# Kernel tuning notes

Measured on AMD Instinct MI355X. Metric: run time of the kernel, lower is better.

## Reference

```python
import jax, jax.numpy as jnp
import numpy as np
from jax import lax

N = 50000          # fluid particles
E = 1_600_000      # radius-graph edges (avg degree 32)
F_IN = 4           # fluidFeatures
NB = 8             # n = m = 8 basis functions per axis
K = NB * NB        # 64 total basis functions
SUPPORT = 1.0      # attributes['support']
LAYERS = [32, 64, 64, 2]


def setup_inputs() -> dict:
    key = jax.random.key(0)
    ks = jax.random.split(key, 24)
    inp = {
        "fluidPositions": jax.random.uniform(ks[0], (N, 2), jnp.float32),
        "fluidFeatures": jax.random.normal(ks[1], (N, F_IN), jnp.float32),
        "edge_i": jax.random.randint(ks[2], (E,), 0, N),  # receiver
        "edge_j": jax.random.randint(ks[3], (E,), 0, N),  # sender
    }
    # conv in/out channels per RbfNet wiring (boundaryFeatures == 0):
    dims = [(F_IN, LAYERS[0]), (2 * LAYERS[0], LAYERS[1]), (LAYERS[1], LAYERS[2]), (LAYERS[2], LAYERS[3])]
    k = 4
    for idx, (ci, co) in enumerate(dims):
        inp[f"cw{idx}"] = 0.1 * jax.random.normal(ks[k], (K, ci, co), jnp.float32); k += 1
        inp[f"cb{idx}"] = jnp.zeros((co,), jnp.float32)
        inp[f"fw{idx}"] = 0.1 * jax.random.normal(ks[k], (ci, co), jnp.float32); k += 1
        inp[f"fb{idx}"] = jnp.zeros((co,), jnp.float32)
    return inp


def _linear_basis(x, n):
    # hat (linear) RBF basis on n uniformly spaced centers in [-1, 1]
    centers = jnp.linspace(-1.0, 1.0, n, dtype=x.dtype)
    spacing = 2.0 / (n - 1)
    return jnp.maximum(0.0, 1.0 - jnp.abs(x[:, None] - centers[None, :]) / spacing)  # [E, n]


def _edge_basis(pos, ei, ej):
    # fluidEdgeLengths = -(pos[j] - pos[i]) / support, clamped to [-1, 1]
    d = (pos[ei] - pos[ej]) / SUPPORT
    d = jnp.clip(d, -1.0, 1.0)
    mask = ei != ej  # centerIgnore: drop self edges
    d = jnp.where(mask[:, None], d, jnp.array([1.0, 0.0], d.dtype))  # keep atan2 grads finite
    r = jnp.sqrt(jnp.sum(d * d, axis=-1) + 1e-12)
    u = jnp.clip(2.0 * r - 1.0, -1.0, 1.0)          # polar mapping: radius -> [-1, 1]
    v = jnp.arctan2(d[:, 1], d[:, 0]) / jnp.pi       # polar mapping: angle  -> [-1, 1]
    bu = _linear_basis(u, NB)
    bv = _linear_basis(v, NB)
    basis = (bu[:, :, None] * bv[:, None, :]).reshape(ei.shape[0], K)  # separable 2D basis
    return basis * mask[:, None].astype(basis.dtype)


def _rbf_conv(x, ei, ej, basis, W, b):
    # out[i] = sum_{e: dst(e)=i} sum_k basis[e,k] * (x[src(e)] @ W[k]) + b
    xj = x[ej]                           # [E, Cin] neighbor gather
    n_nodes = x.shape[0]
    init = jnp.zeros((n_nodes, W.shape[-1]), x.dtype)
    def body(acc, kw):
        bk, Wk = kw                      # bk: [E], Wk: [Cin, Cout]
        mom = jax.ops.segment_sum(bk[:, None] * xj, ei, num_segments=n_nodes)  # [N, Cin]
        return acc + mom @ Wk, None
    out, _ = lax.scan(body, init, (basis.T, W))
    return out + b


def reference(fluidPositions, fluidFeatures, edge_i, edge_j,
              cw0, cb0, fw0, fb0, cw1, cb1, fw1, fb1,
              cw2, cb2, fw2, fb2, cw3, cb3, fw3, fb3):
    basis = _edge_basis(fluidPositions, edge_i, edge_j)
    # layer 0: dense branch + fluid continuous conv, hstacked
    lin0 = fluidFeatures @ fw0 + fb0
    conv0 = _rbf_conv(fluidFeatures, edge_i, edge_j, basis, cw0, cb0)
    ans = jnp.concatenate([lin0, conv0], axis=1)  # [N, 64]
    # layer 1: features 32 != 64 -> no residual
    a = jax.nn.relu(ans)
    ans = _rbf_conv(a, edge_i, edge_j, basis, cw1, cb1) + a @ fw1 + fb1
    # layer 2: features 64 == 64 -> residual add
    a = jax.nn.relu(ans)
    ans = _rbf_conv(a, edge_i, edge_j, basis, cw2, cb2) + a @ fw2 + fb2 + ans
    # layer 3: features 64 != 2 -> no residual
    a = jax.nn.relu(ans)
    ans = _rbf_conv(a, edge_i, edge_j, basis, cw3, cb3) + a @ fw3 + fb3
    return ans / 128.0
```

## Files before the change

### kernel.cpp

```cpp
#include <hip/hip_runtime.h>
#include <math.h>

typedef _Float16 h8 __attribute__((ext_vector_type(8)));
typedef _Float16 h2 __attribute__((ext_vector_type(2)));
typedef float f32x4 __attribute__((ext_vector_type(4)));

__device__ __forceinline__ float clampf(float x, float lo, float hi) {
    return fminf(fmaxf(x, lo), hi);
}

__global__ void zero_ints(int* __restrict__ p, int n) {
    int i = blockIdx.x * 256 + threadIdx.x;
    if (i < n) p[i] = 0;
}

__global__ void repack_wh(const float* __restrict__ cw, const float* __restrict__ fw,
                          _Float16* __restrict__ Wh) {
    int idx = blockIdx.x * 256 + threadIdx.x;
    int total = 4 * 130 * 512;
    if (idx >= total) return;
    int j8 = idx & 7;
    int l = (idx >> 3) & 63;
    int rest = idx >> 9;
    int s = rest % 130;
    int t = rest / 130;
    int p = s * 32 + ((l >> 4) * 8) + j8;
    int co = t * 16 + (l & 15);
    float v = 0.f;
    if (p < 4096) {
        int tile = p >> 8;
        int g = (p >> 6) & 3;
        int m = (p >> 2) & 15;
        int i = p & 3;
        int mt = tile >> 2;
        int ct = tile & 3;
        int bin = mt * 16 + g * 4 + i;
        int c = ct * 16 + m;
        v = cw[(bin * 64 + c) * 64 + co];
    } else if (p < 4160) {
        v = fw[(p - 4096) * 64 + co];
    }
    Wh[idx] = (_Float16)v;
}

__global__ void edge_hist(const int* __restrict__ ei, const int* __restrict__ ej,
                          int* __restrict__ counts, int E) {
    int e = blockIdx.x * 256 + threadIdx.x;
    if (e >= E) return;
    int i = ei[e], j = ej[e];
    if (i != j) atomicAdd(&counts[i], 1);
}

__global__ __launch_bounds__(1024) void scan_kernel(const int* __restrict__ counts,
                                                    int* __restrict__ offs,
                                                    int* __restrict__ cursor, int N) {
    __shared__ int sums[1024];
    const int t = threadIdx.x;
    const int per = (N + 1023) / 1024;
    const int lo = t * per;
    const int hi = min(lo + per, N);
    int s = 0;
    for (int i = lo; i < hi; ++i) s += counts[i];
    sums[t] = s;
    __syncthreads();
    for (int d = 1; d < 1024; d <<= 1) {
        int v = (t >= d) ? sums[t - d] : 0;
        __syncthreads();
        sums[t] += v;
        __syncthreads();
    }
    int run = (t > 0) ? sums[t - 1] : 0;
    for (int i = lo; i < hi; ++i) {
        offs[i] = run;
        cursor[i] = run;
        run += counts[i];
    }
    if (t == 1023) offs[N] = sums[1023];
}

__global__ void edge_scatter(const int* __restrict__ ei, const int* __restrict__ ej,
                             const float* __restrict__ pos, int* __restrict__ cursor,
                             uint4* __restrict__ csr_all, int E) {
    int e = blockIdx.x * 256 + threadIdx.x;
    if (e >= E) return;
    int i = ei[e], j = ej[e];
    if (i == j) return;
    float dx = clampf(pos[i * 2 + 0] - pos[j * 2 + 0], -1.f, 1.f);
    float dy = clampf(pos[i * 2 + 1] - pos[j * 2 + 1], -1.f, 1.f);
    float r = sqrtf(dx * dx + dy * dy + 1e-12f);
    float u = clampf(2.f * r - 1.f, -1.f, 1.f);
    float v = atan2f(dy, dx) * 0.3183098861837907f;
    float tu = (u + 1.f) * 3.5f;
    float tv = (v + 1.f) * 3.5f;
    int iu = min(6, max(0, (int)floorf(tu)));
    int iv = min(6, max(0, (int)floorf(tv)));
    float fu = clampf(tu - (float)iu, 0.f, 1.f);
    float fv = clampf(tv - (float)iv, 0.f, 1.f);
    bool even = (iu & 1) == 0;
    int rowi0 = even ? iu : iu + 1;
    int rowi1 = even ? iu + 1 : iu;
    float wu0 = even ? (1.f - fu) : fu;
    float wu1 = even ? fu : (1.f - fu);
    float gv = 1.f - fv;
    int ivd = iv >> 1;
    unsigned o0 = (unsigned)(rowi0 * 256 + ivd * 64);
    unsigned o1 = (unsigned)(rowi1 * 256 + ivd * 64);
    unsigned offp = o0 | (o1 << 11) | ((unsigned)(iv & 1) << 22);
    unsigned a0 = (unsigned)__builtin_bit_cast(unsigned short, (_Float16)(wu0 * gv)) |
                  ((unsigned)__builtin_bit_cast(unsigned short, (_Float16)(wu0 * fv)) << 16);
    unsigned a1 = (unsigned)__builtin_bit_cast(unsigned short, (_Float16)(wu1 * gv)) |
                  ((unsigned)__builtin_bit_cast(unsigned short, (_Float16)(wu1 * fv)) << 16);
    int p = atomicAdd(&cursor[i], 1);
    csr_all[p] = make_uint4(
        (unsigned)j | ((unsigned)(rowi0 >> 1) << 17) | ((unsigned)(rowi1 >> 1) << 19) |
            ((unsigned)iv << 21),
        offp, a0, a1);
}

template <int MODE>
__global__ __launch_bounds__(1024, 4) void conv64_mfma(
    const _Float16* __restrict__ xh, const float* __restrict__ x32,
    const _Float16* __restrict__ Wh,
    const float* __restrict__ cb, const float* __restrict__ fb,
    const int* __restrict__ offs, const uint4* __restrict__ csr_all,
    float* __restrict__ out32, _Float16* __restrict__ xh_out, int nNodes) {
    constexpr int TM = 16;
    constexpr int KSTEPS = 130;
    constexpr int RSH = 4168;
    extern __shared__ _Float16 smem[];
    const int tid = threadIdx.x;
    const int w = tid >> 6;
    const int lane = tid & 63;
    const int base = blockIdx.x * TM;
    const int n = base + w;

    _Float16* Ast = smem + w * RSH;
    _Float16* Bst = Ast + 2048;

    f32x4 acc[16] = {{0, 0, 0, 0}, {0, 0, 0, 0}, {0, 0, 0, 0}, {0, 0, 0, 0},
                     {0, 0, 0, 0}, {0, 0, 0, 0}, {0, 0, 0, 0}, {0, 0, 0, 0},
                     {0, 0, 0, 0}, {0, 0, 0, 0}, {0, 0, 0, 0}, {0, 0, 0, 0},
                     {0, 0, 0, 0}, {0, 0, 0, 0}, {0, 0, 0, 0}, {0, 0, 0, 0}};

    if (n < nNodes) {
        const int e0 = offs[n], e1 = offs[n + 1];
        const int half = lane >> 5;
        const int el = lane & 31;
        for (int bs = e0; bs < e1; bs += 32) {
            {
                uint4 z4 = make_uint4(0, 0, 0, 0);
#pragma unroll
                for (int zz = 0; zz < 4; ++zz) ((uint4*)Ast)[zz * 64 + lane] = z4;
            }
            int e = bs + el;
            bool ok = e < e1;
            uint4 ca = csr_all[ok ? e : e0];
            int jme = ok ? (int)(ca.x & 0x1FFFF) : -1;
            {
                int iv = (ca.x >> 21) & 7;
                int rowi = half ? (int)((((ca.x >> 19) & 3) << 1) + 1)
                                : (int)(((ca.x >> 17) & 3) << 1);
                h2 wts = __builtin_bit_cast(h2, half ? ca.w : ca.z);
                if (ok) {
                    int bin0 = rowi * 8 + iv;
                    int bin1 = bin0 + 1;
                    int a0 = bin0 * 32 + (((el >> 3) + (bin0 >> 1)) & 3) * 8 + (el & 7);
                    int a1 = bin1 * 32 + (((el >> 3) + (bin1 >> 1)) & 3) * 8 + (el & 7);
                    Ast[a0] = wts[0];
                    Ast[a1] = wts[1];
                }
            }
#pragma unroll
            for (int it = 0; it < 4; ++it) {
                int ee = it * 8 + (lane >> 3);
                int jj = __shfl(jme, ee);
                int c0 = (lane & 7) * 8;
                uint4 bv = make_uint4(0, 0, 0, 0);
                if (jj >= 0) bv = *(const uint4*)(xh + (size_t)jj * 64 + c0);
                int sub = (ee >> 2) * 4 + (c0 >> 4);
                int row = (ee & 3) ^ it;
                ((uint4*)Bst)[sub * 8 + row * 2 + ((c0 >> 3) & 1)] = bv;
            }
            h8 bf[4];
#pragma unroll
            for (int ct = 0; ct < 4; ++ct) {
                h8 b;
#pragma unroll
                for (int jj2 = 0; jj2 < 8; ++jj2) {
                    int ee = (lane >> 4) * 8 + jj2;
                    int addr = ((ee >> 2) * 4 + ct) * 64 + ((ee & 3) ^ (lane >> 4)) * 16 +
                               (lane & 15);
                    b[jj2] = Bst[addr];
                }
                bf[ct] = b;
            }
#pragma unroll
            for (int mt = 0; mt < 4; ++mt) {
                int binr = mt * 16 + (lane & 15);
                int aoff = binr * 32 + (((lane >> 4) + (binr >> 1)) & 3) * 8;
                h8 a = *(const h8*)(Ast + aoff);
#pragma unroll
                for (int ct = 0; ct < 4; ++ct)
                    acc[mt * 4 + ct] = __builtin_amdgcn_mfma_f32_16x16x32_f16(
                        a, bf[ct], acc[mt * 4 + ct], 0, 0, 0);
            }
        }
#pragma unroll
        for (int t = 0; t < 16; ++t) {
            h2 lo = {(_Float16)acc[t][0], (_Float16)acc[t][1]};
            h2 hi = {(_Float16)acc[t][2], (_Float16)acc[t][3]};
            h2* dst = (h2*)(smem + w * RSH + t * 256 + (lane >> 4) * 64 + (lane & 15) * 4);
            dst[0] = lo;
            dst[1] = hi;
        }
        smem[w * RSH + 4096 + lane] = xh[(size_t)n * 64 + lane];
    }

    const int s0 = w * 8 + min(w, 2);
    const int s_end = s0 + 8 + (w < 2 ? 1 : 0);
    const int quad = lane >> 4;
    const _Float16* arow = smem + (lane & 15) * RSH;

    const uint4* Bp = (const uint4*)Wh;
    uint4 b0[4], b1[4];
#pragma unroll
    for (int t = 0; t < 4; ++t) {
        b0[t] = Bp[((size_t)t * KSTEPS + s0) * 64 + lane];
        b1[t] = Bp[((size_t)t * KSTEPS + s0 + 1) * 64 + lane];
    }
    __syncthreads();
    f32x4 acc2[4] = {{0, 0, 0, 0}, {0, 0, 0, 0}, {0, 0, 0, 0}, {0, 0, 0, 0}};
    for (int s = s0; s < s_end; ++s) {
        uint4 bq[4];
#pragma unroll
        for (int t = 0; t < 4; ++t) {
            bq[t] = b0[t];
            b0[t] = b1[t];
            if (s + 2 < s_end) b1[t] = Bp[((size_t)t * KSTEPS + s + 2) * 64 + lane];
        }
        h8 a = *(const h8*)(arow + s * 32 + quad * 8);
#pragma unroll
        for (int t = 0; t < 4; ++t)
            acc2[t] = __builtin_amdgcn_mfma_f32_16x16x32_f16(a, __builtin_bit_cast(h8, bq[t]),
                                                             acc2[t], 0, 0, 0);
    }
    __syncthreads();
    f32x4* red = (f32x4*)smem;
#pragma unroll
    for (int t = 0; t < 4; ++t) red[(w * 4 + t) * 64 + lane] = acc2[t];
    __syncthreads();
    if (w < 4) {
        f32x4 s = {0, 0, 0, 0};
#pragma unroll
        for (int g = 0; g < 16; ++g) s += red[(g * 4 + w) * 64 + lane];
        const int co = w * 16 + (lane & 15);
#pragma unroll
        for (int i = 0; i < 4; ++i) {
            int nn = base + quad * 4 + i;
            if (nn < nNodes) {
                float res = s[i] + cb[co] + fb[co];
                if (MODE == 2) res += x32[(size_t)nn * 64 + co];
                out32[(size_t)nn * 64 + co] = res;
                if (MODE == 1) xh_out[(size_t)nn * 64 + co] = (_Float16)fmaxf(res, 0.f);
            }
        }
    }
}

__global__ __launch_bounds__(1024, 4) void conv_last(
    const float* __restrict__ x, const float* __restrict__ cw3, const float* __restrict__ fw3,
    const float* __restrict__ cb3, const float* __restrict__ fb3,
    const int* __restrict__ offs, const uint4* __restrict__ csr_all,
    float* __restrict__ out, int nNodes) {
    constexpr int TM = 16;
    __shared__ float2 W2[4096];
    __shared__ float2 FW2[64];
    const int tid = threadIdx.x;
    const int w = tid >> 6;
    const int lane = tid & 63;
    const int base = blockIdx.x * TM;
    const int n = base + w;

    {
        const float2* src = (const float2*)cw3;
        for (int d = tid; d < 4096; d += 1024) W2[d] = src[d];
        if (tid < 64) FW2[tid] = ((const float2*)fw3)[tid];
    }
    __syncthreads();

    float2 acc = make_float2(0.f, 0.f);
    if (n < nNodes) {
        const int e0 = offs[n], e1 = offs[n + 1];
        const int c = lane;
        for (int b = e0; b < e1; b += 4) {
            uint4 ca[4];
            float xv[4];
#pragma unroll
            for (int u = 0; u < 4; ++u) {
                int e = b + u;
                bool ok = e < e1;
                ca[u] = csr_all[ok ? e : e0];
                xv[u] = ok ? 1.f : 0.f;
            }
#pragma unroll
            for (int u = 0; u < 4; ++u) {
                int j = ca[u].x & 0x1FFFF;
                xv[u] *= fmaxf(x[j * 64 + c], 0.f);
            }
#pragma unroll
            for (int u = 0; u < 4; ++u) {
                int r0 = ((ca[u].x >> 17) & 3) << 1;
                int r1 = (((ca[u].x >> 19) & 3) << 1) + 1;
                int iv = (ca[u].x >> 21) & 7;
                h2 wh0 = __builtin_bit_cast(h2, ca[u].z);
                h2 wh1 = __builtin_bit_cast(h2, ca[u].w);
                float w00 = (float)wh0[0], w01 = (float)wh0[1];
                float w10 = (float)wh1[0], w11 = (float)wh1[1];
                int b00 = (r0 * 8 + iv) * 64 + c;
                int b10 = (r1 * 8 + iv) * 64 + c;
                float2 t00 = W2[b00], t01 = W2[b00 + 64];
                float2 t10 = W2[b10], t11 = W2[b10 + 64];
                float wsx = w00 * t00.x + w01 * t01.x + w10 * t10.x + w11 * t11.x;
                float wsy = w00 * t00.y + w01 * t01.y + w10 * t10.y + w11 * t11.y;
                acc.x += xv[u] * wsx;
                acc.y += xv[u] * wsy;
            }
        }
        float xr = fmaxf(x[n * 64 + c], 0.f);
        float2 fwp = FW2[c];
        acc.x += xr * fwp.x;
        acc.y += xr * fwp.y;
    }
#pragma unroll
    for (int d = 1; d < 64; d <<= 1) {
        acc.x += __shfl_xor(acc.x, d);
        acc.y += __shfl_xor(acc.y, d);
    }
    if (lane == 0 && n < nNodes) {
        out[n * 2 + 0] = (acc.x + cb3[0] + fb3[0]) * (1.f / 128.f);
        out[n * 2 + 1] = (acc.y + cb3[1] + fb3[1]) * (1.f / 128.f);
    }
}

__global__ __launch_bounds__(1024, 4) void conv0_direct(
    const float* __restrict__ x, const float* __restrict__ cw0, const float* __restrict__ fw0,
    const float* __restrict__ cb0, const float* __restrict__ fb0,
    const int* __restrict__ offs, const uint4* __restrict__ csr_all,
    _Float16* __restrict__ out, int nNodes) {
    constexpr int TM = 16;
    __shared__ float2 W0p[4096];
    __shared__ float2 FW0p[64];
    const int tid = threadIdx.x;
    const int w = tid >> 6;
    const int lane = tid & 63;
    const int base = blockIdx.x * TM;
    const int n = base + w;

    {
        for (int d = tid; d < 4096; d += 1024) {
            int co = d & 31;
            int h = (d >> 5) & 1;
            int bin = d >> 6;
            W0p[d] = make_float2(cw0[(bin * 4 + 2 * h) * 32 + co],
                                 cw0[(bin * 4 + 2 * h + 1) * 32 + co]);
        }
        if (tid < 64) {
            int co = tid & 31;
            int h = tid >> 5;
            FW0p[tid] = make_float2(fw0[(2 * h) * 32 + co], fw0[(2 * h + 1) * 32 + co]);
        }
    }
    __syncthreads();

    const int co = lane & 31;
    const int h = lane >> 5;
    float accC = 0.f, accL = 0.f;
    if (n < nNodes) {
        const int e0 = offs[n], e1 = offs[n + 1];
        for (int b = e0; b < e1; b += 4) {
            uint4 ca[4];
            float xc0[4], xc1[4];
#pragma unroll
            for (int u = 0; u < 4; ++u) {
                int e = b + u;
                bool ok = e < e1;
                ca[u] = csr_all[ok ? e : e0];
                xc0[u] = ok ? 1.f : 0.f;
            }
#pragma unroll
            for (int u = 0; u < 4; ++u) {
                int j = ca[u].x & 0x1FFFF;
                const float4 xj = *(const float4*)(x + j * 4);
                float a = h ? xj.z : xj.x;
                float bb = h ? xj.w : xj.y;
                xc1[u] = xc0[u] * bb;
                xc0[u] = xc0[u] * a;
            }
#pragma unroll
            for (int u = 0; u < 4; ++u) {
                int r0 = ((ca[u].x >> 17) & 3) << 1;
                int r1 = (((ca[u].x >> 19) & 3) << 1) + 1;
                int iv = (ca[u].x >> 21) & 7;
                h2 wh0 = __builtin_bit_cast(h2, ca[u].z);
                h2 wh1 = __builtin_bit_cast(h2, ca[u].w);
                float w00 = (float)wh0[0], w01 = (float)wh0[1];
                float w10 = (float)wh1[0], w11 = (float)wh1[1];
                int i00 = ((r0 * 8 + iv) * 2 + h) * 32 + co;
                int i10 = ((r1 * 8 + iv) * 2 + h) * 32 + co;
                float2 t00 = W0p[i00], t01 = W0p[i00 + 64];
                float2 t10 = W0p[i10], t11 = W0p[i10 + 64];
                accC += w00 * (xc0[u] * t00.x + xc1[u] * t00.y);
                accC += w01 * (xc0[u] * t01.x + xc1[u] * t01.y);
                accC += w10 * (xc0[u] * t10.x + xc1[u] * t10.y);
                accC += w11 * (xc0[u] * t11.x + xc1[u] * t11.y);
            }
        }
        const float4 xn = *(const float4*)(x + n * 4);
        float a = h ? xn.z : xn.x;
        float bb = h ? xn.w : xn.y;
        float2 fwp = FW0p[h * 32 + co];
        accL = a * fwp.x + bb * fwp.y;
    }
    accC += __shfl_xor(accC, 32);
    accL += __shfl_xor(accL, 32);
    if (lane < 32 && n < nNodes) {
        out[n * 64 + co] = (_Float16)fmaxf(accL + fb0[co], 0.f);
        out[n * 64 + 32 + co] = (_Float16)fmaxf(accC + cb0[co], 0.f);
    }
}

extern "C" void kernel_launch(void* const* d_in, const int* in_sizes, int n_in,
                              void* d_out, int out_size, void* d_ws, size_t ws_size,
                              hipStream_t stream) {
    const float* pos = (const float*)d_in[0];
    const float* feat = (const float*)d_in[1];
    const int* ei = (const int*)d_in[2];
    const int* ej = (const int*)d_in[3];
    const float* cw0 = (const float*)d_in[4];
    const float* cb0 = (const float*)d_in[5];
    const float* fw0 = (const float*)d_in[6];
    const float* fb0 = (const float*)d_in[7];
    const float* cw1 = (const float*)d_in[8];
    const float* cb1 = (const float*)d_in[9];
    const float* fw1 = (const float*)d_in[10];
    const float* fb1 = (const float*)d_in[11];
    const float* cw2 = (const float*)d_in[12];
    const float* cb2 = (const float*)d_in[13];
    const float* fw2 = (const float*)d_in[14];
    const float* fb2 = (const float*)d_in[15];
    const float* cw3 = (const float*)d_in[16];
    const float* cb3 = (const float*)d_in[17];
    const float* fw3 = (const float*)d_in[18];
    const float* fb3 = (const float*)d_in[19];
    float* outp = (float*)d_out;

    const int N = in_sizes[0] / 2;
    const int E = in_sizes[2];

    char* wsp = (char*)d_ws;
    size_t off = 0;
    auto alloc = [&](size_t bytes) -> void* {
        void* p = wsp + off;
        off = (off + bytes + 255) & ~(size_t)255;
        return p;
    };
    int* counts = (int*)alloc((size_t)N * 4);
    int* offs = (int*)alloc((size_t)(N + 1) * 4);
    int* cursor = (int*)alloc((size_t)N * 4);
    uint4* csr_all = (uint4*)alloc((size_t)E * 16);
    float* ansA = (float*)alloc((size_t)N * 64 * 4);
    float* ansB = (float*)alloc((size_t)N * 64 * 4);
    _Float16* xhB = (_Float16*)alloc((size_t)N * 64 * 2);
    _Float16* Wh1 = (_Float16*)alloc((size_t)4 * 130 * 512 * 2);
    _Float16* Wh2 = (_Float16*)alloc((size_t)4 * 130 * 512 * 2);
    _Float16* xh0 = (_Float16*)ansA;
    (void)ws_size;
    (void)n_in;
    (void)out_size;

    const int BIG_LDS = 16 * 4168 * 2;
    hipFuncSetAttribute((const void*)&conv64_mfma<1>,
                        hipFuncAttributeMaxDynamicSharedMemorySize, BIG_LDS);
    hipFuncSetAttribute((const void*)&conv64_mfma<2>,
                        hipFuncAttributeMaxDynamicSharedMemorySize, BIG_LDS);

    zero_ints<<<dim3((N + 255) / 256), dim3(256), 0, stream>>>(counts, N);
    const int RT = 4 * 130 * 512;
    repack_wh<<<dim3((RT + 255) / 256), dim3(256), 0, stream>>>(cw1, fw1, Wh1);
    repack_wh<<<dim3((RT + 255) / 256), dim3(256), 0, stream>>>(cw2, fw2, Wh2);
    edge_hist<<<dim3((E + 255) / 256), dim3(256), 0, stream>>>(ei, ej, counts, E);
    scan_kernel<<<dim3(1), dim3(1024), 0, stream>>>(counts, offs, cursor, N);
    edge_scatter<<<dim3((E + 255) / 256), dim3(256), 0, stream>>>(ei, ej, pos, cursor, csr_all, E);

    const int nb = (N + 15) / 16;
    conv0_direct<<<dim3(nb), dim3(1024), 0, stream>>>(
        feat, cw0, fw0, cb0, fb0, offs, csr_all, xh0, N);
    conv64_mfma<1><<<dim3(nb), dim3(1024), BIG_LDS, stream>>>(
        xh0, (const float*)nullptr, Wh1, cb1, fb1, offs, csr_all, ansB, xhB, N);
    conv64_mfma<2><<<dim3(nb), dim3(1024), BIG_LDS, stream>>>(
        xhB, ansB, Wh2, cb2, fb2, offs, csr_all, ansA, (_Float16*)nullptr, N);
    conv_last<<<dim3(nb), dim3(1024), 0, stream>>>(
        ansA, cw3, fw3, cb3, fb3, offs, csr_all, outp, N);
}
```

Before: 915.3 us.

## Move first and last conv layers onto MFMA gather-then-GEMM path

Replaces the scalar direct-accumulation kernels for layer 0 and the final layer with MFMA-based kernels. Each builds per-node basis moments in LDS via matrix ops, then multiplies by repacked fp16 weights, with a block-level reduction across waves. Layer 2 now emits fp16 post-ReLU activations instead of fp32, so the last layer gathers half the bytes per neighbour. The edge record drops its unused offset word. In exchange the final layer runs in fp16 with mostly-padded 16-wide output tiles, and two more weight repack launches are added.

Measured after the change: 856.8 us. 6.4% less time.

```diff
diff --git a/kernel.cpp b/kernel.cpp
--- a/kernel.cpp
+++ b/kernel.cpp
@@ -43,6 +43,59 @@
     Wh[idx] = (_Float16)v;
 }
 
+__global__ void repack_wh3(const float* __restrict__ cw, const float* __restrict__ fw,
+                           _Float16* __restrict__ Wh) {
+    int idx = blockIdx.x * 256 + threadIdx.x;
+    int total = 130 * 512;
+    if (idx >= total) return;
+    int j8 = idx & 7;
+    int l = (idx >> 3) & 63;
+    int s = idx >> 9;
+    int p = s * 32 + ((l >> 4) * 8) + j8;
+    int co = l & 15;
+    float v = 0.f;
+    if (co < 2) {
+        if (p < 4096) {
+            int tile = p >> 8;
+            int g = (p >> 6) & 3;
+            int m = (p >> 2) & 15;
+            int i = p & 3;
+            int mt = tile >> 2;
+            int ct = tile & 3;
+            int bin = mt * 16 + g * 4 + i;
+            int c = ct * 16 + m;
+            v = cw[(bin * 64 + c) * 2 + co];
+        } else if (p < 4160) {
+            v = fw[(p - 4096) * 2 + co];
+        }
+    }
+    Wh[idx] = (_Float16)v;
+}
+
+__global__ void repack_w0h(const float* __restrict__ cw0, const float* __restrict__ fw0,
+                           _Float16* __restrict__ Wh) {
+    int idx = blockIdx.x * 256 + threadIdx.x;
+    int total = 4 * 9 * 512;
+    if (idx >= total) return;
+    int j8 = idx & 7;
+    int l = (idx >> 3) & 63;
+    int rest = idx >> 9;
+    int s = rest % 9;
+    int t = rest / 9;
+    int p = s * 32 + ((l >> 4) * 8) + j8;
+    int co = t * 16 + (l & 15);
+    float v = 0.f;
+    if (p < 256) {
+        int bin = p & 63;
+        int c = p >> 6;
+        if (co >= 32) v = cw0[(bin * 4 + c) * 32 + (co - 32)];
+    } else if (p < 260) {
+        int c = p - 256;
+        if (co < 32) v = fw0[c * 32 + co];
+    }
+    Wh[idx] = (_Float16)v;
+}
+
 __global__ void edge_hist(const int* __restrict__ ei, const int* __restrict__ ej,
                           int* __restrict__ counts, int E) {
     int e = blockIdx.x * 256 + threadIdx.x;
@@ -102,10 +155,6 @@
     float wu0 = even ? (1.f - fu) : fu;
     float wu1 = even ? fu : (1.f - fu);
     float gv = 1.f - fv;
-    int ivd = iv >> 1;
-    unsigned o0 = (unsigned)(rowi0 * 256 + ivd * 64);
-    unsigned o1 = (unsigned)(rowi1 * 256 + ivd * 64);
-    unsigned offp = o0 | (o1 << 11) | ((unsigned)(iv & 1) << 22);
     unsigned a0 = (unsigned)__builtin_bit_cast(unsigned short, (_Float16)(wu0 * gv)) |
                   ((unsigned)__builtin_bit_cast(unsigned short, (_Float16)(wu0 * fv)) << 16);
     unsigned a1 = (unsigned)__builtin_bit_cast(unsigned short, (_Float16)(wu1 * gv)) |
@@ -114,7 +163,85 @@
     csr_all[p] = make_uint4(
         (unsigned)j | ((unsigned)(rowi0 >> 1) << 17) | ((unsigned)(rowi1 >> 1) << 19) |
             ((unsigned)iv << 21),
-        offp, a0, a1);
+        0u, a0, a1);
+}
+
+__device__ __forceinline__ void mom_phase1_64(
+    const _Float16* __restrict__ xh, const uint4* __restrict__ csr_all,
+    _Float16* Ast, _Float16* Bst, int e0, int e1, int lane, f32x4* acc) {
+    const int half = lane >> 5;
+    const int el = lane & 31;
+    for (int bs = e0; bs < e1; bs += 32) {
+        {
+            uint4 z4 = make_uint4(0, 0, 0, 0);
+#pragma unroll
+            for (int zz = 0; zz < 4; ++zz) ((uint4*)Ast)[zz * 64 + lane] = z4;
+        }
+        int e = bs + el;
+        bool ok = e < e1;
+        uint4 ca = csr_all[ok ? e : e0];
+        int jme = ok ? (int)(ca.x & 0x1FFFF) : -1;
+        {
+            int iv = (ca.x >> 21) & 7;
+            int rowi = half ? (int)((((ca.x >> 19) & 3) << 1) + 1)
+                            : (int)(((ca.x >> 17) & 3) << 1);
+            h2 wts = __builtin_bit_cast(h2, half ? ca.w : ca.z);
+            if (ok) {
+                int bin0 = rowi * 8 + iv;
+                int bin1 = bin0 + 1;
+                int a0 = bin0 * 32 + (((el >> 3) + (bin0 >> 1)) & 3) * 8 + (el & 7);
+                int a1 = bin1 * 32 + (((el >> 3) + (bin1 >> 1)) & 3) * 8 + (el & 7);
+                Ast[a0] = wts[0];
+                Ast[a1] = wts[1];
+            }
+        }
+#pragma unroll
+        for (int it = 0; it < 4; ++it) {
+            int ee = it * 8 + (lane >> 3);
+            int jj = __shfl(jme, ee);
+            int c0 = (lane & 7) * 8;
+            uint4 bv = make_uint4(0, 0, 0, 0);
+            if (jj >= 0) bv = *(const uint4*)(xh + (size_t)jj * 64 + c0);
+            int sub = (ee >> 2) * 4 + (c0 >> 4);
+            int row = (ee & 3) ^ it;
+            ((uint4*)Bst)[sub * 8 + row * 2 + ((c0 >> 3) & 1)] = bv;
+        }
+        h8 bf[4];
+#pragma unroll
+        for (int ct = 0; ct < 4; ++ct) {
+            h8 b;
+#pragma unroll
+            for (int jj2 = 0; jj2 < 8; ++jj2) {
+                int ee = (lane >> 4) * 8 + jj2;
+                int addr = ((ee >> 2) * 4 + ct) * 64 + ((ee & 3) ^ (lane >> 4)) * 16 +
+                           (lane & 15);
+                b[jj2] = Bst[addr];
+            }
+            bf[ct] = b;
+        }
+#pragma unroll
+        for (int mt = 0; mt < 4; ++mt) {
+            int binr = mt * 16 + (lane & 15);
+            int aoff = binr * 32 + (((lane >> 4) + (binr >> 1)) & 3) * 8;
+            h8 a = *(const h8*)(Ast + aoff);
+#pragma unroll
+            for (int ct = 0; ct < 4; ++ct)
+                acc[mt * 4 + ct] = __builtin_amdgcn_mfma_f32_16x16x32_f16(
+                    a, bf[ct], acc[mt * 4 + ct], 0, 0, 0);
+        }
+    }
+}
+
+__device__ __forceinline__ void mom_writeback_64(const f32x4* acc, _Float16* momrow,
+                                                 int lane) {
+#pragma unroll
+    for (int t = 0; t < 16; ++t) {
+        h2 lo = {(_Float16)acc[t][0], (_Float16)acc[t][1]};
+        h2 hi = {(_Float16)acc[t][2], (_Float16)acc[t][3]};
+        h2* dst = (h2*)(momrow + t * 256 + (lane >> 4) * 64 + (lane & 15) * 4);
+        dst[0] = lo;
+        dst[1] = hi;
+    }
 }
 
 template <int MODE>
@@ -126,7 +253,7 @@
     float* __restrict__ out32, _Float16* __restrict__ xh_out, int nNodes) {
     constexpr int TM = 16;
     constexpr int KSTEPS = 130;
-    constexpr int RSH = 4168;
+    constexpr int RSH = 4184;
     extern __shared__ _Float16 smem[];
     const int tid = threadIdx.x;
     const int w = tid >> 6;
@@ -141,6 +268,146 @@
                      {0, 0, 0, 0}, {0, 0, 0, 0}, {0, 0, 0, 0}, {0, 0, 0, 0},
                      {0, 0, 0, 0}, {0, 0, 0, 0}, {0, 0, 0, 0}, {0, 0, 0, 0},
                      {0, 0, 0, 0}, {0, 0, 0, 0}, {0, 0, 0, 0}, {0, 0, 0, 0}};
+
+    if (n < nNodes) {
+        mom_phase1_64(xh, csr_all, Ast, Bst, offs[n], offs[n + 1], lane, acc);
+        mom_writeback_64(acc, smem + w * RSH, lane);
+        smem[w * RSH + 4096 + lane] = xh[(size_t)n * 64 + lane];
+    }
+
+    const int s0 = w * 8 + min(w, 2);
+    const int s_end = s0 + 8 + (w < 2 ? 1 : 0);
+    const int quad = lane >> 4;
+    const _Float16* arow = smem + (lane & 15) * RSH;
+
+    const uint4* Bp = (const uint4*)Wh;
+    uint4 b0[4], b1[4];
+#pragma unroll
+    for (int t = 0; t < 4; ++t) {
+        b0[t] = Bp[((size_t)t * KSTEPS + s0) * 64 + lane];
+        b1[t] = Bp[((size_t)t * KSTEPS + s0 + 1) * 64 + lane];
+    }
+    __syncthreads();
+    f32x4 acc2[4] = {{0, 0, 0, 0}, {0, 0, 0, 0}, {0, 0, 0, 0}, {0, 0, 0, 0}};
+    for (int s = s0; s < s_end; ++s) {
+        uint4 bq[4];
+#pragma unroll
+        for (int t = 0; t < 4; ++t) {
+            bq[t] = b0[t];
+            b0[t] = b1[t];
+            if (s + 2 < s_end) b1[t] = Bp[((size_t)t * KSTEPS + s + 2) * 64 + lane];
+        }
+        h8 a = *(const h8*)(arow + s * 32 + quad * 8);
+#pragma unroll
+        for (int t = 0; t < 4; ++t)
+            acc2[t] = __builtin_amdgcn_mfma_f32_16x16x32_f16(a, __builtin_bit_cast(h8, bq[t]),
+                                                             acc2[t], 0, 0, 0);
+    }
+    __syncthreads();
+    f32x4* red = (f32x4*)smem;
+#pragma unroll
+    for (int t = 0; t < 4; ++t) red[(w * 4 + t) * 64 + lane] = acc2[t];
+    __syncthreads();
+    if (w < 4) {
+        f32x4 s = {0, 0, 0, 0};
+#pragma unroll
+        for (int g = 0; g < 16; ++g) s += red[(g * 4 + w) * 64 + lane];
+        const int co = w * 16 + (lane & 15);
+#pragma unroll
+        for (int i = 0; i < 4; ++i) {
+            int nn = base + quad * 4 + i;
+            if (nn < nNodes) {
+                float res = s[i] + cb[co] + fb[co];
+                if (MODE == 2) res += x32[(size_t)nn * 64 + co];
+                if (MODE == 1) out32[(size_t)nn * 64 + co] = res;
+                xh_out[(size_t)nn * 64 + co] = (_Float16)fmaxf(res, 0.f);
+            }
+        }
+    }
+}
+
+__global__ __launch_bounds__(1024, 4) void conv_last_mfma(
+    const _Float16* __restrict__ xh, const _Float16* __restrict__ Wh3,
+    const float* __restrict__ cb3, const float* __restrict__ fb3,
+    const int* __restrict__ offs, const uint4* __restrict__ csr_all,
+    float* __restrict__ out, int nNodes) {
+    constexpr int TM = 16;
+    constexpr int RSH = 4184;
+    extern __shared__ _Float16 smem[];
+    const int tid = threadIdx.x;
+    const int w = tid >> 6;
+    const int lane = tid & 63;
+    const int base = blockIdx.x * TM;
+    const int n = base + w;
+
+    _Float16* Ast = smem + w * RSH;
+    _Float16* Bst = Ast + 2048;
+
+    f32x4 acc[16] = {{0, 0, 0, 0}, {0, 0, 0, 0}, {0, 0, 0, 0}, {0, 0, 0, 0},
+                     {0, 0, 0, 0}, {0, 0, 0, 0}, {0, 0, 0, 0}, {0, 0, 0, 0},
+                     {0, 0, 0, 0}, {0, 0, 0, 0}, {0, 0, 0, 0}, {0, 0, 0, 0},
+                     {0, 0, 0, 0}, {0, 0, 0, 0}, {0, 0, 0, 0}, {0, 0, 0, 0}};
+
+    if (n < nNodes) {
+        mom_phase1_64(xh, csr_all, Ast, Bst, offs[n], offs[n + 1], lane, acc);
+        mom_writeback_64(acc, smem + w * RSH, lane);
+        smem[w * RSH + 4096 + lane] = xh[(size_t)n * 64 + lane];
+    }
+
+    const int s0 = w * 8 + min(w, 2);
+    const int s_end = s0 + 8 + (w < 2 ? 1 : 0);
+    const int quad = lane >> 4;
+    const _Float16* arow = smem + (lane & 15) * RSH;
+    const uint4* Bp = (const uint4*)Wh3;
+
+    __syncthreads();
+    f32x4 acc2 = {0, 0, 0, 0};
+    for (int s = s0; s < s_end; ++s) {
+        uint4 bq = Bp[(size_t)s * 64 + lane];
+        h8 a = *(const h8*)(arow + s * 32 + quad * 8);
+        acc2 = __builtin_amdgcn_mfma_f32_16x16x32_f16(a, __builtin_bit_cast(h8, bq),
+                                                      acc2, 0, 0, 0);
+    }
+    __syncthreads();
+    f32x4* red = (f32x4*)smem;
+    red[w * 64 + lane] = acc2;
+    __syncthreads();
+    if (w == 0) {
+        f32x4 s = {0, 0, 0, 0};
+#pragma unroll
+        for (int g = 0; g < 16; ++g) s += red[g * 64 + lane];
+        const int co = lane & 15;
+        if (co < 2) {
+#pragma unroll
+            for (int i = 0; i < 4; ++i) {
+                int nn = base + quad * 4 + i;
+                if (nn < nNodes)
+                    out[nn * 2 + co] = (s[i] + cb3[co] + fb3[co]) * (1.f / 128.f);
+            }
+        }
+    }
+}
+
+__global__ __launch_bounds__(1024, 4) void conv0_mfma(
+    const float* __restrict__ xf, const _Float16* __restrict__ W0h,
+    const float* __restrict__ cb0, const float* __restrict__ fb0,
+    const int* __restrict__ offs, const uint4* __restrict__ csr_all,
+    _Float16* __restrict__ xh_out, int nNodes) {
+    constexpr int TM = 16;
+    constexpr int RSH0 = 296;
+    constexpr int MOMSZ = 16 * RSH0;
+    extern __shared__ _Float16 smem[];
+    const int tid = threadIdx.x;
+    const int w = tid >> 6;
+    const int lane = tid & 63;
+    const int base = blockIdx.x * TM;
+    const int n = base + w;
+
+    _Float16* Ast = smem + MOMSZ + w * 2560;
+    _Float16* Bst = Ast + 2048;
+    _Float16* momrow = smem + w * RSH0;
+
+    f32x4 acc[4] = {{0, 0, 0, 0}, {0, 0, 0, 0}, {0, 0, 0, 0}, {0, 0, 0, 0}};
 
     if (n < nNodes) {
         const int e0 = offs[n], e1 = offs[n + 1];
@@ -170,74 +437,58 @@
                     Ast[a1] = wts[1];
                 }
             }
-#pragma unroll
-            for (int it = 0; it < 4; ++it) {
-                int ee = it * 8 + (lane >> 3);
-                int jj = __shfl(jme, ee);
-                int c0 = (lane & 7) * 8;
-                uint4 bv = make_uint4(0, 0, 0, 0);
-                if (jj >= 0) bv = *(const uint4*)(xh + (size_t)jj * 64 + c0);
-                int sub = (ee >> 2) * 4 + (c0 >> 4);
-                int row = (ee & 3) ^ it;
-                ((uint4*)Bst)[sub * 8 + row * 2 + ((c0 >> 3) & 1)] = bv;
-            }
-            h8 bf[4];
-#pragma unroll
-            for (int ct = 0; ct < 4; ++ct) {
-                h8 b;
-#pragma unroll
-                for (int jj2 = 0; jj2 < 8; ++jj2) {
-                    int ee = (lane >> 4) * 8 + jj2;
-                    int addr = ((ee >> 2) * 4 + ct) * 64 + ((ee & 3) ^ (lane >> 4)) * 16 +
-                               (lane & 15);
-                    b[jj2] = Bst[addr];
-                }
-                bf[ct] = b;
+            if (half == 0) {
+                float4 xj = make_float4(0.f, 0.f, 0.f, 0.f);
+                if (jme >= 0) xj = *(const float4*)(xf + (size_t)jme * 4);
+                h2 d0 = {(_Float16)xj.x, (_Float16)xj.y};
+                h2 d1 = {(_Float16)xj.z, (_Float16)xj.w};
+                uint4 bv = make_uint4(__builtin_bit_cast(unsigned, d0),
+                                      __builtin_bit_cast(unsigned, d1), 0u, 0u);
+                uint4* dst = (uint4*)Bst + (el >> 2) * 8 + (el & 3) * 2;
+                dst[0] = bv;
+                dst[1] = make_uint4(0, 0, 0, 0);
+            }
+            h8 b;
+#pragma unroll
+            for (int jj2 = 0; jj2 < 8; ++jj2) {
+                int ee = (lane >> 4) * 8 + jj2;
+                b[jj2] = Bst[(ee >> 2) * 64 + (ee & 3) * 16 + (lane & 15)];
             }
 #pragma unroll
             for (int mt = 0; mt < 4; ++mt) {
                 int binr = mt * 16 + (lane & 15);
                 int aoff = binr * 32 + (((lane >> 4) + (binr >> 1)) & 3) * 8;
                 h8 a = *(const h8*)(Ast + aoff);
-#pragma unroll
-                for (int ct = 0; ct < 4; ++ct)
-                    acc[mt * 4 + ct] = __builtin_amdgcn_mfma_f32_16x16x32_f16(
-                        a, bf[ct], acc[mt * 4 + ct], 0, 0, 0);
-            }
-        }
-#pragma unroll
-        for (int t = 0; t < 16; ++t) {
-            h2 lo = {(_Float16)acc[t][0], (_Float16)acc[t][1]};
-            h2 hi = {(_Float16)acc[t][2], (_Float16)acc[t][3]};
-            h2* dst = (h2*)(smem + w * RSH + t * 256 + (lane >> 4) * 64 + (lane & 15) * 4);
-            dst[0] = lo;
-            dst[1] = hi;
-        }
-        smem[w * RSH + 4096 + lane] = xh[(size_t)n * 64 + lane];
-    }
-
-    const int s0 = w * 8 + min(w, 2);
-    const int s_end = s0 + 8 + (w < 2 ? 1 : 0);
+                acc[mt] = __builtin_amdgcn_mfma_f32_16x16x32_f16(a, b, acc[mt], 0, 0, 0);
+            }
+        }
+        if ((lane & 15) < 4) {
+#pragma unroll
+            for (int mt = 0; mt < 4; ++mt) {
+                _Float16* dst = momrow + mt * 16 + (lane >> 4) * 4 + 64 * (lane & 15);
+                ((h2*)dst)[0] = h2{(_Float16)acc[mt][0], (_Float16)acc[mt][1]};
+                ((h2*)dst)[1] = h2{(_Float16)acc[mt][2], (_Float16)acc[mt][3]};
+            }
+        }
+        if (lane < 7) {
+            h2 z = {(_Float16)0.f, (_Float16)0.f};
+            h2* zp = (h2*)(momrow + 260 + lane * 4);
+            zp[0] = z;
+            zp[1] = z;
+        }
+        if (lane < 4) momrow[256 + lane] = (_Float16)xf[(size_t)n * 4 + lane];
+    }
+
     const int quad = lane >> 4;
-    const _Float16* arow = smem + (lane & 15) * RSH;
-
-    const uint4* Bp = (const uint4*)Wh;
-    uint4 b0[4], b1[4];
-#pragma unroll
-    for (int t = 0; t < 4; ++t) {
-        b0[t] = Bp[((size_t)t * KSTEPS + s0) * 64 + lane];
-        b1[t] = Bp[((size_t)t * KSTEPS + s0 + 1) * 64 + lane];
-    }
+    const _Float16* arow = smem + (lane & 15) * RSH0;
+    const uint4* Bp = (const uint4*)W0h;
     __syncthreads();
     f32x4 acc2[4] = {{0, 0, 0, 0}, {0, 0, 0, 0}, {0, 0, 0, 0}, {0, 0, 0, 0}};
+    const int s0 = min(w, 9), s_end = min(w + 1, 9);
     for (int s = s0; s < s_end; ++s) {
         uint4 bq[4];
 #pragma unroll
-        for (int t = 0; t < 4; ++t) {
-            bq[t] = b0[t];
-            b0[t] = b1[t];
-            if (s + 2 < s_end) b1[t] = Bp[((size_t)t * KSTEPS + s + 2) * 64 + lane];
-        }
+        for (int t = 0; t < 4; ++t) bq[t] = Bp[((size_t)t * 9 + s) * 64 + lane];
         h8 a = *(const h8*)(arow + s * 32 + quad * 8);
 #pragma unroll
         for (int t = 0; t < 4; ++t)
@@ -245,7 +496,7 @@
                                                              acc2[t], 0, 0, 0);
     }
     __syncthreads();
-    f32x4* red = (f32x4*)smem;
+    f32x4* red = (f32x4*)(smem + MOMSZ);
 #pragma unroll
     for (int t = 0; t < 4; ++t) red[(w * 4 + t) * 64 + lane] = acc2[t];
     __syncthreads();
@@ -254,178 +505,13 @@
 #pragma unroll
         for (int g = 0; g < 16; ++g) s += red[(g * 4 + w) * 64 + lane];
         const int co = w * 16 + (lane & 15);
+        const float bias = (co < 32) ? fb0[co] : cb0[co - 32];
 #pragma unroll
         for (int i = 0; i < 4; ++i) {
             int nn = base + quad * 4 + i;
-            if (nn < nNodes) {
-                float res = s[i] + cb[co] + fb[co];
-                if (MODE == 2) res += x32[(size_t)nn * 64 + co];
-                out32[(size_t)nn * 64 + co] = res;
-                if (MODE == 1) xh_out[(size_t)nn * 64 + co] = (_Float16)fmaxf(res, 0.f);
-            }
-        }
-    }
-}
-
-__global__ __launch_bounds__(1024, 4) void conv_last(
-    const float* __restrict__ x, const float* __restrict__ cw3, const float* __restrict__ fw3,
-    const float* __restrict__ cb3, const float* __restrict__ fb3,
-    const int* __restrict__ offs, const uint4* __restrict__ csr_all,
-    float* __restrict__ out, int nNodes) {
-    constexpr int TM = 16;
-    __shared__ float2 W2[4096];
-    __shared__ float2 FW2[64];
-    const int tid = threadIdx.x;
-    const int w = tid >> 6;
-    const int lane = tid & 63;
-    const int base = blockIdx.x * TM;
-    const int n = base + w;
-
-    {
-        const float2* src = (const float2*)cw3;
-        for (int d = tid; d < 4096; d += 1024) W2[d] = src[d];
-        if (tid < 64) FW2[tid] = ((const float2*)fw3)[tid];
-    }
-    __syncthreads();
-
-    float2 acc = make_float2(0.f, 0.f);
-    if (n < nNodes) {
-        const int e0 = offs[n], e1 = offs[n + 1];
-        const int c = lane;
-        for (int b = e0; b < e1; b += 4) {
-            uint4 ca[4];
-            float xv[4];
-#pragma unroll
-            for (int u = 0; u < 4; ++u) {
-                int e = b + u;
-                bool ok = e < e1;
-                ca[u] = csr_all[ok ? e : e0];
-                xv[u] = ok ? 1.f : 0.f;
-            }
-#pragma unroll
-            for (int u = 0; u < 4; ++u) {
-                int j = ca[u].x & 0x1FFFF;
-                xv[u] *= fmaxf(x[j * 64 + c], 0.f);
-            }
-#pragma unroll
-            for (int u = 0; u < 4; ++u) {
-                int r0 = ((ca[u].x >> 17) & 3) << 1;
-                int r1 = (((ca[u].x >> 19) & 3) << 1) + 1;
-                int iv = (ca[u].x >> 21) & 7;
-                h2 wh0 = __builtin_bit_cast(h2, ca[u].z);
-                h2 wh1 = __builtin_bit_cast(h2, ca[u].w);
-                float w00 = (float)wh0[0], w01 = (float)wh0[1];
-                float w10 = (float)wh1[0], w11 = (float)wh1[1];
-                int b00 = (r0 * 8 + iv) * 64 + c;
-                int b10 = (r1 * 8 + iv) * 64 + c;
-                float2 t00 = W2[b00], t01 = W2[b00 + 64];
-                float2 t10 = W2[b10], t11 = W2[b10 + 64];
-                float wsx = w00 * t00.x + w01 * t01.x + w10 * t10.x + w11 * t11.x;
-                float wsy = w00 * t00.y + w01 * t01.y + w10 * t10.y + w11 * t11.y;
-                acc.x += xv[u] * wsx;
-                acc.y += xv[u] * wsy;
-            }
-        }
-        float xr = fmaxf(x[n * 64 + c], 0.f);
-        float2 fwp = FW2[c];
-        acc.x += xr * fwp.x;
-        acc.y += xr * fwp.y;
-    }
-#pragma unroll
-    for (int d = 1; d < 64; d <<= 1) {
-        acc.x += __shfl_xor(acc.x, d);
-        acc.y += __shfl_xor(acc.y, d);
-    }
-    if (lane == 0 && n < nNodes) {
-        out[n * 2 + 0] = (acc.x + cb3[0] + fb3[0]) * (1.f / 128.f);
-        out[n * 2 + 1] = (acc.y + cb3[1] + fb3[1]) * (1.f / 128.f);
-    }
-}
-
-__global__ __launch_bounds__(1024, 4) void conv0_direct(
-    const float* __restrict__ x, const float* __restrict__ cw0, const float* __restrict__ fw0,
-    const float* __restrict__ cb0, const float* __restrict__ fb0,
-    const int* __restrict__ offs, const uint4* __restrict__ csr_all,
-    _Float16* __restrict__ out, int nNodes) {
-    constexpr int TM = 16;
-    __shared__ float2 W0p[4096];
-    __shared__ float2 FW0p[64];
-    const int tid = threadIdx.x;
-    const int w = tid >> 6;
-    const int lane = tid & 63;
-    const int base = blockIdx.x * TM;
-    const int n = base + w;
-
-    {
-        for (int d = tid; d < 4096; d += 1024) {
-            int co = d & 31;
-            int h = (d >> 5) & 1;
-            int bin = d >> 6;
-            W0p[d] = make_float2(cw0[(bin * 4 + 2 * h) * 32 + co],
-                                 cw0[(bin * 4 + 2 * h + 1) * 32 + co]);
-        }
-        if (tid < 64) {
-            int co = tid & 31;
-            int h = tid >> 5;
-            FW0p[tid] = make_float2(fw0[(2 * h) * 32 + co], fw0[(2 * h + 1) * 32 + co]);
-        }
-    }
-    __syncthreads();
-
-    const int co = lane & 31;
-    const int h = lane >> 5;
-    float accC = 0.f, accL = 0.f;
-    if (n < nNodes) {
-        const int e0 = offs[n], e1 = offs[n + 1];
-        for (int b = e0; b < e1; b += 4) {
-            uint4 ca[4];
-            float xc0[4], xc1[4];
-#pragma unroll
-            for (int u = 0; u < 4; ++u) {
-                int e = b + u;
-                bool ok = e < e1;
-                ca[u] = csr_all[ok ? e : e0];
-                xc0[u] = ok ? 1.f : 0.f;
-            }
-#pragma unroll
-            for (int u = 0; u < 4; ++u) {
-                int j = ca[u].x & 0x1FFFF;
-                const float4 xj = *(const float4*)(x + j * 4);
-                float a = h ? xj.z : xj.x;
-                float bb = h ? xj.w : xj.y;
-                xc1[u] = xc0[u] * bb;
-                xc0[u] = xc0[u] * a;
-            }
-#pragma unroll
-            for (int u = 0; u < 4; ++u) {
-                int r0 = ((ca[u].x >> 17) & 3) << 1;
-                int r1 = (((ca[u].x >> 19) & 3) << 1) + 1;
-                int iv = (ca[u].x >> 21) & 7;
-                h2 wh0 = __builtin_bit_cast(h2, ca[u].z);
-                h2 wh1 = __builtin_bit_cast(h2, ca[u].w);
-                float w00 = (float)wh0[0], w01 = (float)wh0[1];
-                float w10 = (float)wh1[0], w11 = (float)wh1[1];
-                int i00 = ((r0 * 8 + iv) * 2 + h) * 32 + co;
-                int i10 = ((r1 * 8 + iv) * 2 + h) * 32 + co;
-                float2 t00 = W0p[i00], t01 = W0p[i00 + 64];
-                float2 t10 = W0p[i10], t11 = W0p[i10 + 64];
-                accC += w00 * (xc0[u] * t00.x + xc1[u] * t00.y);
-                accC += w01 * (xc0[u] * t01.x + xc1[u] * t01.y);
-                accC += w10 * (xc0[u] * t10.x + xc1[u] * t10.y);
-                accC += w11 * (xc0[u] * t11.x + xc1[u] * t11.y);
-            }
-        }
-        const float4 xn = *(const float4*)(x + n * 4);
-        float a = h ? xn.z : xn.x;
-        float bb = h ? xn.w : xn.y;
-        float2 fwp = FW0p[h * 32 + co];
-        accL = a * fwp.x + bb * fwp.y;
-    }
-    accC += __shfl_xor(accC, 32);
-    accL += __shfl_xor(accL, 32);
-    if (lane < 32 && n < nNodes) {
-        out[n * 64 + co] = (_Float16)fmaxf(accL + fb0[co], 0.f);
-        out[n * 64 + 32 + co] = (_Float16)fmaxf(accC + cb0[co], 0.f);
+            if (nn < nNodes)
+                xh_out[(size_t)nn * 64 + co] = (_Float16)fmaxf(s[i] + bias, 0.f);
+        }
     }
 }
 
@@ -468,37 +554,46 @@
     int* offs = (int*)alloc((size_t)(N + 1) * 4);
     int* cursor = (int*)alloc((size_t)N * 4);
     uint4* csr_all = (uint4*)alloc((size_t)E * 16);
-    float* ansA = (float*)alloc((size_t)N * 64 * 4);
     float* ansB = (float*)alloc((size_t)N * 64 * 4);
+    _Float16* xh0 = (_Float16*)alloc((size_t)N * 64 * 2);
     _Float16* xhB = (_Float16*)alloc((size_t)N * 64 * 2);
+    _Float16* xhC = (_Float16*)alloc((size_t)N * 64 * 2);
     _Float16* Wh1 = (_Float16*)alloc((size_t)4 * 130 * 512 * 2);
     _Float16* Wh2 = (_Float16*)alloc((size_t)4 * 130 * 512 * 2);
-    _Float16* xh0 = (_Float16*)ansA;
+    _Float16* Wh3 = (_Float16*)alloc((size_t)130 * 512 * 2);
+    _Float16* W0h = (_Float16*)alloc((size_t)4 * 9 * 512 * 2);
     (void)ws_size;
     (void)n_in;
     (void)out_size;
 
-    const int BIG_LDS = 16 * 4168 * 2;
+    const int BIG_LDS = 16 * 4184 * 2;
+    const int LDS0 = (16 * 296 + 16 * 2560) * 2;
     hipFuncSetAttribute((const void*)&conv64_mfma<1>,
                         hipFuncAttributeMaxDynamicSharedMemorySize, BIG_LDS);
     hipFuncSetAttribute((const void*)&conv64_mfma<2>,
                         hipFuncAttributeMaxDynamicSharedMemorySize, BIG_LDS);
+    hipFuncSetAttribute((const void*)&conv_last_mfma,
+                        hipFuncAttributeMaxDynamicSharedMemorySize, BIG_LDS);
+    hipFuncSetAttribute((const void*)&conv0_mfma,
+                        hipFuncAttributeMaxDynamicSharedMemorySize, LDS0);
 
     zero_ints<<<dim3((N + 255) / 256), dim3(256), 0, stream>>>(counts, N);
     const int RT = 4 * 130 * 512;
     repack_wh<<<dim3((RT + 255) / 256), dim3(256), 0, stream>>>(cw1, fw1, Wh1);
     repack_wh<<<dim3((RT + 255) / 256), dim3(256), 0, stream>>>(cw2, fw2, Wh2);
+    repack_wh3<<<dim3((130 * 512 + 255) / 256), dim3(256), 0, stream>>>(cw3, fw3, Wh3);
+    repack_w0h<<<dim3((4 * 9 * 512 + 255) / 256), dim3(256), 0, stream>>>(cw0, fw0, W0h);
     edge_hist<<<dim3((E + 255) / 256), dim3(256), 0, stream>>>(ei, ej, counts, E);
     scan_kernel<<<dim3(1), dim3(1024), 0, stream>>>(counts, offs, cursor, N);
     edge_scatter<<<dim3((E + 255) / 256), dim3(256), 0, stream>>>(ei, ej, pos, cursor, csr_all, E);
 
     const int nb = (N + 15) / 16;
-    conv0_direct<<<dim3(nb), dim3(1024), 0, stream>>>(
-        feat, cw0, fw0, cb0, fb0, offs, csr_all, xh0, N);
+    conv0_mfma<<<dim3(nb), dim3(1024), LDS0, stream>>>(
+        feat, W0h, cb0, fb0, offs, csr_all, xh0, N);
     conv64_mfma<1><<<dim3(nb), dim3(1024), BIG_LDS, stream>>>(
         xh0, (const float*)nullptr, Wh1, cb1, fb1, offs, csr_all, ansB, xhB, N);
     conv64_mfma<2><<<dim3(nb), dim3(1024), BIG_LDS, stream>>>(
-        xhB, ansB, Wh2, cb2, fb2, offs, csr_all, ansA, (_Float16*)nullptr, N);
-    conv_last<<<dim3(nb), dim3(1024), 0, stream>>>(
-        ansA, cw3, fw3, cb3, fb3, offs, csr_all, outp, N);
-}
+        xhB, ansB, Wh2, cb2, fb2, offs, csr_all, (float*)nullptr, xhC, N);
+    conv_last_mfma<<<dim3(nb), dim3(1024), BIG_LDS, stream>>>(
+        xhC, Wh3, cb3, fb3, offs, csr_all, outp, N);
+}
```
